# Kernel optimization log

Measured on AMD Instinct MI355X. Metric: run time of the kernel, lower is better.

The kernel has to match this reference:

```python
import jax, jax.numpy as jnp
import numpy as np

B, V, K = 128, 128000, 20
_SAMPLING_EPS = 1e-5


def setup_inputs() -> dict:
    key = jax.random.key(0)
    k1, k2, k3 = jax.random.split(key, 3)
    logits = jax.random.normal(k1, (B, V), dtype=jnp.float32)
    temp = jax.random.uniform(k2, (B,), dtype=jnp.float32, minval=0.2, maxval=1.5)
    # every 4th sequence is greedy (temperature < eps)
    temp = jnp.where(jnp.arange(B) % 4 == 0, 0.0, temp)
    # uniform noise in (0,1); exponential noise is q = -log(u)
    u = jax.random.uniform(k3, (B, V), dtype=jnp.float32, minval=1e-7, maxval=1.0)
    return {"logits": logits, "temp": temp, "u": u, "max_num_logprobs": K}


def reference(logits, temp, u, max_num_logprobs):
    # apply_temperature: greedy rows (temp < eps) use temp=1.0
    t = jnp.where(temp < _SAMPLING_EPS, 1.0, temp)
    scaled = logits.astype(jnp.float32) / t[:, None]          # [B, V]
    probs = jax.nn.softmax(scaled, axis=-1)                    # [B, V]
    # greedy sample
    greedy = jnp.argmax(probs, axis=1)                         # [B]
    # random sample via exponential-race (Gumbel-max equivalent): argmax(probs / Exp(1))
    q = -jnp.log(u)                                            # Exp(1) noise
    random_sampled = jnp.argmax(probs / q, axis=1)             # [B]
    sampled = jnp.where(temp < _SAMPLING_EPS, greedy, random_sampled)
    # top-k logprobs
    logprobs = jax.nn.log_softmax(scaled, axis=-1)             # [B, V]
    topk_logprobs, topk_indices = jax.lax.top_k(logprobs, max_num_logprobs)
    return sampled, topk_logprobs, topk_indices
```

## Files before the change

kernel.cpp:

```cpp
#include <hip/hip_runtime.h>
#include <stdint.h>


#define KMAX 20
#define SAMPLING_EPS 1e-5f
#define TAU 3.0f
#define CPB 64
#define LOG2E 1.44269504f
#define SMARGIN 3e-4f
#define TILE 256

static __device__ __forceinline__ float fexp2(float x) {
#if __has_builtin(__builtin_amdgcn_exp2f)
    return __builtin_amdgcn_exp2f(x);
#else
    return exp2f(x);
#endif
}

static __device__ __forceinline__ unsigned int ord32(float v) {
    unsigned int u = __float_as_uint(v);
    return u ^ ((unsigned int)((int)u >> 31) | 0x80000000u);
}
static __device__ __forceinline__ float unord32(unsigned int x) {
    unsigned int u = (x & 0x80000000u) ? (x ^ 0x80000000u) : ~x;
    return __uint_as_float(u);
}
static __device__ __forceinline__ unsigned long long shflxor64(unsigned long long v, int off) {
    int lo = __shfl_xor((int)(unsigned int)v, off, 64);
    int hi = __shfl_xor((int)(unsigned int)(v >> 32), off, 64);
    return ((unsigned long long)(unsigned int)hi << 32) | (unsigned int)lo;
}

static __device__ __forceinline__ float gumbel_exact(float x, float inv_t, float uu, float wm) {
    const float q = (uu > 0.984375f) ? -log1pf(-wm) : -__logf(uu);
    return x * inv_t - __logf(q);
}

static __device__ __forceinline__ float gub_bound(float a, float uu) {
    return fmaf((float)__float_as_uint(1.0f - uu), -0x1p-23f, 127.0f + a);
}

static __device__ __forceinline__ void g2lds(const float4* gaddr, float4* lds_wave_base, int lane) {
#if __has_builtin(__builtin_amdgcn_global_load_lds)
    __builtin_amdgcn_global_load_lds(
        (const __attribute__((address_space(1))) void*)gaddr,
        (__attribute__((address_space(3))) void*)lds_wave_base, 16, 0, 0);
#else
    lds_wave_base[lane] = *gaddr;
#endif
}

__global__ __launch_bounds__(256, 8) void k1_partials(
        const float* __restrict__ logits, const float* __restrict__ u,
        const float* __restrict__ temp,
        unsigned int* __restrict__ wrec,
        unsigned int* __restrict__ cntbuf,
        uint2* __restrict__ candbuf,
        int V, int nsplit) {
    __shared__ float4 sL[2][TILE];
    __shared__ float4 sU[2][TILE];
    __shared__ int cnt;
    __shared__ uint2 cand[CPB];
    const int b = blockIdx.x;
    const int t = threadIdx.x;
    const int lane = t & 63;
    const int w = t >> 6;
    if (t == 0) cnt = 0;

    const int nrows = gridDim.x / nsplit;
    const int mb = b % nrows;
    const int sp = b / nrows;
    int r = (mb * 61 + (sp >> 1)) % nrows;
    if ((nrows & (nrows - 1)) == 0) r ^= (r >> 4);
    const int slot = r * nsplit + sp;

    const float traw = temp[r];
    const bool greedy = traw < SAMPLING_EPS;
    const float inv_t = greedy ? 1.0f : (1.0f / traw);
    const float it2 = inv_t * LOG2E;

    const int nf4 = V >> 2;
    const int per = (nf4 + nsplit - 1) / nsplit;
    const int f0 = sp * per;
    const int f1 = min(f0 + per, nf4);
    const int len = f1 - f0;
    const int ntiles = (len + TILE - 1) / TILE;

    const float4* __restrict__ l4 = (const float4*)(logits + (size_t)r * V);
    const float4* __restrict__ u4 = (const float4*)(u + (size_t)r * V);

    float s0 = 0.0f, s1 = 0.0f, s2 = 0.0f, s3 = 0.0f;
    float gv = -INFINITY;
    int gcol = 0;
    float gvs2 = INFINITY;
    const float4 z4 = make_float4(0.f, 0.f, 0.f, 0.f);

#define STAGE(bb, tt) do { \
        const int si_ = f0 + (tt) * TILE + t; \
        if (si_ < f1) { \
            g2lds(l4 + si_, &sL[bb][w * 64], lane); \
            if (!greedy) g2lds(u4 + si_, &sU[bb][w * 64], lane); \
        } \
    } while (0)

#define PUSH(xv, cc) do { \
        const int pi_ = atomicAdd(&cnt, 1); \
        if (pi_ < CPB) cand[pi_] = make_uint2(__float_as_uint(xv), (unsigned)(cc)); \
    } while (0)

    STAGE(0, 0);
    if (ntiles > 1) STAGE(1, 1);

    for (int k = 0; k < ntiles; ++k) {
        __syncthreads();
        const int idx = f0 + k * TILE + t;
        const bool act = idx < f1;
        const int cur = k & 1;
        float4 la = z4, ua = z4;
        if (act) {
            la = sL[cur][t];
            if (!greedy) ua = sU[cur][t];
        }
        __syncthreads();
        if (k + 2 < ntiles) STAGE(cur, k + 2);

        if (greedy) {
            if (act) {
                s0 += fexp2(la.x * it2); s1 += fexp2(la.y * it2);
                s2 += fexp2(la.z * it2); s3 += fexp2(la.w * it2);
                const float xm = fmaxf(fmaxf(la.x, la.y), fmaxf(la.z, la.w));
                if (xm >= TAU) {
                    const int c0 = idx << 2;
                    if (la.x >= TAU) PUSH(la.x, c0);
                    if (la.y >= TAU) PUSH(la.y, c0 + 1);
                    if (la.z >= TAU) PUSH(la.z, c0 + 2);
                    if (la.w >= TAU) PUSH(la.w, c0 + 3);
                }
            }
        } else if (k == 0) {
            if (act) {
                const int c0 = idx << 2;
                s0 += fexp2(la.x * it2); s1 += fexp2(la.y * it2);
                s2 += fexp2(la.z * it2); s3 += fexp2(la.w * it2);
                { const float g = gumbel_exact(la.x, inv_t, ua.x, 1.0f - ua.x);
                  if (g > gv) { gv = g; gcol = c0; } }
                { const float g = gumbel_exact(la.y, inv_t, ua.y, 1.0f - ua.y);
                  if (g > gv) { gv = g; gcol = c0 + 1; } }
                { const float g = gumbel_exact(la.z, inv_t, ua.z, 1.0f - ua.z);
                  if (g > gv) { gv = g; gcol = c0 + 2; } }
                { const float g = gumbel_exact(la.w, inv_t, ua.w, 1.0f - ua.w);
                  if (g > gv) { gv = g; gcol = c0 + 3; } }
                const float xm = fmaxf(fmaxf(la.x, la.y), fmaxf(la.z, la.w));
                if (xm >= TAU) {
                    if (la.x >= TAU) PUSH(la.x, c0);
                    if (la.y >= TAU) PUSH(la.y, c0 + 1);
                    if (la.z >= TAU) PUSH(la.z, c0 + 2);
                    if (la.w >= TAU) PUSH(la.w, c0 + 3);
                }
            }
            float gmax = gv;
            #pragma unroll
            for (int off = 1; off < 64; off <<= 1) gmax = fmaxf(gmax, __shfl_xor(gmax, off, 64));
            gvs2 = fmaf(gmax, LOG2E, -SMARGIN);
        } else if (act) {
#define EX(gj, xv, uu, cc) \
            if ((gj) > gvs2) { \
                const float wm_ = 1.0f - (uu); \
                const float ge_ = gumbel_exact(xv, inv_t, uu, wm_); \
                if (ge_ > gv) { gv = ge_; gcol = (cc); gvs2 = fmaf(ge_, LOG2E, -SMARGIN); } \
            }
            const int c0 = idx << 2;
            const float a0 = la.x * it2, a1 = la.y * it2, a2 = la.z * it2, a3 = la.w * it2;
            s0 += fexp2(a0); s1 += fexp2(a1); s2 += fexp2(a2); s3 += fexp2(a3);
            const float g0 = gub_bound(a0, ua.x), g1 = gub_bound(a1, ua.y);
            const float g2 = gub_bound(a2, ua.z), g3 = gub_bound(a3, ua.w);
            const float gm = fmaxf(fmaxf(g0, g1), fmaxf(g2, g3));
            if (gm > gvs2) {
                EX(g0, la.x, ua.x, c0)
                EX(g1, la.y, ua.y, c0 + 1)
                EX(g2, la.z, ua.z, c0 + 2)
                EX(g3, la.w, ua.w, c0 + 3)
            }
            const float xm = fmaxf(fmaxf(la.x, la.y), fmaxf(la.z, la.w));
            if (xm >= TAU) {
                if (la.x >= TAU) PUSH(la.x, c0);
                if (la.y >= TAU) PUSH(la.y, c0 + 1);
                if (la.z >= TAU) PUSH(la.z, c0 + 2);
                if (la.w >= TAU) PUSH(la.w, c0 + 3);
            }
#undef EX
        }
    }
#undef PUSH
#undef STAGE

    float s = (s0 + s1) + (s2 + s3);
    #pragma unroll
    for (int off = 1; off < 64; off <<= 1) s += __shfl_xor(s, off, 64);
    unsigned long long gk = greedy ? 0ull
        : (((unsigned long long)ord32(gv) << 32) | (unsigned int)~(unsigned int)gcol);
    #pragma unroll
    for (int off = 1; off < 64; off <<= 1) {
        const unsigned long long o = shflxor64(gk, off);
        gk = (o > gk) ? o : gk;
    }
    if (lane == 0) {
        unsigned int* rp = wrec + (size_t)(slot * 4 + w) * 4;
        rp[0] = __float_as_uint(s);
        rp[1] = __float_as_uint(unord32((unsigned int)(gk >> 32)));
        rp[2] = ~(unsigned int)gk;
    }
    __syncthreads();
    const int c = cnt;
    if (t == 0) cntbuf[slot] = (unsigned)c;
    if (t < min(c, CPB)) candbuf[(size_t)slot * CPB + t] = cand[t];
}

__global__ __launch_bounds__(64) void k2_finalize(
        const unsigned int* __restrict__ wrec, const unsigned int* __restrict__ cntbuf,
        const uint2* __restrict__ candbuf, const float* __restrict__ logits,
        const float* __restrict__ temp, float* __restrict__ out,
        int B, int V, int K, int nsplit) {
    __shared__ unsigned long long kbuf[512];
    const int r = blockIdx.x;
    const int lane = threadIdx.x;
    const int NW = nsplit * 4;

    const float traw = temp[r];
    const bool greedy = traw < SAMPLING_EPS;
    const float tt = greedy ? 1.0f : traw;

    float s = 0.0f;
    unsigned long long gk = 0ull;
    if (lane < NW) {
        const unsigned int* rp = wrec + (size_t)(r * NW + lane) * 4;
        s = __uint_as_float(rp[0]);
        gk = ((unsigned long long)ord32(__uint_as_float(rp[1])) << 32) | (unsigned int)~rp[2];
    }
    #pragma unroll
    for (int off = 1; off < 64; off <<= 1) s += __shfl_xor(s, off, 64);
    #pragma unroll
    for (int off = 1; off < 64; off <<= 1) {
        const unsigned long long o = shflxor64(gk, off);
        gk = (o > gk) ? o : gk;
    }
    const float lS = logf(s);

    const int cnt_raw = (lane < nsplit) ? (int)cntbuf[r * nsplit + lane] : 0;
    const int cntc = min(cnt_raw, CPB);
    const bool ovf = __ballot(cnt_raw > CPB) != 0ull;
    int incl = cntc;
    #pragma unroll
    for (int d = 1; d < 64; d <<= 1) {
        const int o = __shfl_up(incl, d, 64);
        if (lane >= d) incl += o;
    }
    const int T = __shfl(incl, 63, 64);
    const int off0 = incl - cntc;

    unsigned long long keys[8];
    #pragma unroll
    for (int jj = 0; jj < 8; ++jj) keys[jj] = 0ull;

    if (!ovf && T >= K && T <= 512) {
        if (lane < nsplit) {
            const uint2* cb = candbuf + (size_t)(r * nsplit + lane) * CPB;
            for (int i = 0; i < cntc; ++i) {
                const uint2 e = cb[i];
                kbuf[off0 + i] = ((unsigned long long)ord32(__uint_as_float(e.x)) << 32)
                               | (unsigned int)~e.y;
            }
        }
        __syncthreads();
        #pragma unroll
        for (int jj = 0; jj < 8; ++jj) {
            const int idx = lane + 64 * jj;
            if (idx < T) keys[jj] = kbuf[idx];
        }
    } else {
        unsigned long long mykey = ((unsigned long long)0x007FFFFFu) << 32;
        unsigned long long minkey = mykey;
        float vmin = -INFINITY;
        const float* lr = logits + (size_t)r * V;
        for (int base = 0; base < V; base += 64) {
            const int i = base + lane;
            const float x = (i < V) ? lr[i] : -INFINITY;
            unsigned long long cm = __ballot((i < V) && (x >= vmin));
            while (cm) {
                const int src = (int)__builtin_ctzll(cm);
                cm &= cm - 1;
                const float cv = __shfl(x, src, 64);
                const int cc = __shfl(i, src, 64);
                const unsigned long long ck =
                    ((unsigned long long)ord32(cv) << 32) | (unsigned int)~(unsigned int)cc;
                if (ck > minkey) {
                    const bool own = (lane < K) && (mykey == minkey);
                    const unsigned long long om = __ballot(own);
                    if (lane == (int)__builtin_ctzll(om)) mykey = ck;
                    unsigned long long mk = (lane < K) ? mykey : ~0ull;
                    #pragma unroll
                    for (int o2 = 1; o2 < 64; o2 <<= 1) {
                        const unsigned long long o = shflxor64(mk, o2);
                        mk = (o < mk) ? o : mk;
                    }
                    minkey = mk;
                    vmin = unord32((unsigned int)(mk >> 32));
                }
            }
        }
        keys[0] = (lane < K) ? mykey : 0ull;
    }

    float* out_s  = out;
    float* out_lp = out + B;
    float* out_ix = out + B + (size_t)B * K;

    unsigned int top1 = 0;
    for (int k = 0; k < K; ++k) {
        unsigned long long loc = keys[0];
        #pragma unroll
        for (int jj = 1; jj < 8; ++jj) loc = (keys[jj] > loc) ? keys[jj] : loc;
        #pragma unroll
        for (int off = 1; off < 64; off <<= 1) {
            const unsigned long long o = shflxor64(loc, off);
            loc = (o > loc) ? o : loc;
        }
        #pragma unroll
        for (int jj = 0; jj < 8; ++jj) if (keys[jj] == loc) keys[jj] = 0ull;
        if (lane == 0) {
            const unsigned int col = ~(unsigned int)loc;
            const float v = unord32((unsigned int)(loc >> 32));
            out_lp[(size_t)r * K + k] = v / tt - lS;
            out_ix[(size_t)r * K + k] = (float)col;
            if (k == 0) top1 = col;
        }
    }
    if (lane == 0) {
        out_s[r] = (float)(greedy ? top1 : (~(unsigned int)gk));
    }
}

extern "C" void kernel_launch(void* const* d_in, const int* in_sizes, int n_in,
                              void* d_out, int out_size, void* d_ws, size_t ws_size,
                              hipStream_t stream) {
    const float* logits = (const float*)d_in[0];
    const float* temp   = (const float*)d_in[1];
    const float* u      = (const float*)d_in[2];
    const int B = in_sizes[1];
    const int V = in_sizes[0] / B;
    int K = (out_size - B) / (2 * B);
    if (K > KMAX) K = KMAX;
    if (K < 1) K = 1;

    int nsplit = 16;
    while (nsplit > 1 && (size_t)B * nsplit * 580 > ws_size) nsplit >>= 1;
    const int blocks = B * nsplit;

    unsigned int* wrec   = (unsigned int*)d_ws;
    unsigned int* cntbuf = wrec + (size_t)blocks * 16;
    uint2*        candbf = (uint2*)(cntbuf + blocks);

    k1_partials<<<dim3(blocks), dim3(256), 0, stream>>>(
        logits, u, temp, wrec, cntbuf, candbf, V, nsplit);
    k2_finalize<<<dim3(B), dim3(64), 0, stream>>>(
        wrec, cntbuf, candbf, logits, temp, (float*)d_out, B, V, K, nsplit);
}
```

Baseline: 163.4 us.

## Replace block barriers with per-wave vmcnt waits in LDS double-buffer loop

The tile loop no longer calls __syncthreads twice per iteration. Each wave stages and consumes only its own 64-slot slice of the shared buffers, so synchronisation is done per wave with explicit s_waitcnt vmcnt counters and sched_barrier fences, and the next prefetch is issued after compute. The aim is to remove block-wide barrier stalls and let waves run independently. The cost is reliance on exact vmcnt accounting; any extra outstanding loads or a mismatch in per-wave tile counts could cause reads of stale LDS data.

Result: no change. 163.9 us (+0.3%).

```diff
diff --git a/kernel.cpp b/kernel.cpp
--- a/kernel.cpp
+++ b/kernel.cpp
@@ -8,7 +8,6 @@
 #define CPB 64
 #define LOG2E 1.44269504f
 #define SMARGIN 3e-4f
-#define TILE 256
 
 static __device__ __forceinline__ float fexp2(float x) {
 #if __has_builtin(__builtin_amdgcn_exp2f)
@@ -58,8 +57,8 @@
         unsigned int* __restrict__ cntbuf,
         uint2* __restrict__ candbuf,
         int V, int nsplit) {
-    __shared__ float4 sL[2][TILE];
-    __shared__ float4 sU[2][TILE];
+    __shared__ float4 sL[2][256];
+    __shared__ float4 sU[2][256];
     __shared__ int cnt;
     __shared__ uint2 cand[CPB];
     const int b = blockIdx.x;
@@ -67,6 +66,7 @@
     const int lane = t & 63;
     const int w = t >> 6;
     if (t == 0) cnt = 0;
+    __syncthreads();
 
     const int nrows = gridDim.x / nsplit;
     const int mb = b % nrows;
@@ -84,11 +84,12 @@
     const int per = (nf4 + nsplit - 1) / nsplit;
     const int f0 = sp * per;
     const int f1 = min(f0 + per, nf4);
-    const int len = f1 - f0;
-    const int ntiles = (len + TILE - 1) / TILE;
 
     const float4* __restrict__ l4 = (const float4*)(logits + (size_t)r * V);
     const float4* __restrict__ u4 = (const float4*)(u + (size_t)r * V);
+
+    const int fw0 = f0 + w * 64;
+    const int nt = (f1 > fw0) ? ((f1 - fw0 + 255) >> 8) : 0;
 
     float s0 = 0.0f, s1 = 0.0f, s2 = 0.0f, s3 = 0.0f;
     float gv = -INFINITY;
@@ -96,11 +97,11 @@
     float gvs2 = INFINITY;
     const float4 z4 = make_float4(0.f, 0.f, 0.f, 0.f);
 
-#define STAGE(bb, tt) do { \
-        const int si_ = f0 + (tt) * TILE + t; \
+#define STAGEJ(jj) do { \
+        const int si_ = f0 + (jj) * 256 + t; \
         if (si_ < f1) { \
-            g2lds(l4 + si_, &sL[bb][w * 64], lane); \
-            if (!greedy) g2lds(u4 + si_, &sU[bb][w * 64], lane); \
+            g2lds(l4 + si_, &sL[(jj) & 1][w * 64], lane); \
+            if (!greedy) g2lds(u4 + si_, &sU[(jj) & 1][w * 64], lane); \
         } \
     } while (0)
 
@@ -109,21 +110,26 @@
         if (pi_ < CPB) cand[pi_] = make_uint2(__float_as_uint(xv), (unsigned)(cc)); \
     } while (0)
 
-    STAGE(0, 0);
-    if (ntiles > 1) STAGE(1, 1);
-
-    for (int k = 0; k < ntiles; ++k) {
-        __syncthreads();
-        const int idx = f0 + k * TILE + t;
+    STAGEJ(0);
+    STAGEJ(1);
+
+    for (int j = 0; j < nt; ++j) {
+        if (j + 1 < nt) {
+            if (greedy) asm volatile("s_waitcnt vmcnt(1)" ::: "memory");
+            else        asm volatile("s_waitcnt vmcnt(2)" ::: "memory");
+        } else {
+            asm volatile("s_waitcnt vmcnt(0)" ::: "memory");
+        }
+        __builtin_amdgcn_sched_barrier(0);
+
+        const int idx = f0 + j * 256 + t;
         const bool act = idx < f1;
-        const int cur = k & 1;
+        const int cur = j & 1;
         float4 la = z4, ua = z4;
         if (act) {
             la = sL[cur][t];
             if (!greedy) ua = sU[cur][t];
         }
-        __syncthreads();
-        if (k + 2 < ntiles) STAGE(cur, k + 2);
 
         if (greedy) {
             if (act) {
@@ -138,7 +144,7 @@
                     if (la.w >= TAU) PUSH(la.w, c0 + 3);
                 }
             }
-        } else if (k == 0) {
+        } else if (j == 0) {
             if (act) {
                 const int c0 = idx << 2;
                 s0 += fexp2(la.x * it2); s1 += fexp2(la.y * it2);
@@ -191,9 +197,12 @@
             }
 #undef EX
         }
+
+        __builtin_amdgcn_sched_barrier(0);
+        STAGEJ(j + 2);
     }
 #undef PUSH
-#undef STAGE
+#undef STAGEJ
 
     float s = (s0 + s1) + (s2 + s3);
     #pragma unroll
```
